# Kernel optimization log

Hardware: AMD Instinct MI355X
Metric: run time of the kernel (lower is better)

Reference implementation:

```python
import jax, jax.numpy as jnp
import numpy as np


def setup_inputs() -> dict:
    key = jax.random.key(0)
    k1, _ = jax.random.split(key)
    x = jax.random.normal(k1, (2, 16, 16, 16, 64), dtype=jnp.float32)
    gamma = jnp.ones((1,), dtype=jnp.float32)  # learned scalar (zeros at init; ones to make output nontrivial)
    return {"x": x, "gamma": gamma}


def reference(x, gamma):
    # x: (B, D, H, W, C); faithful to the Keras layer: flatten spatial dims,
    # energy = Q @ Q^T over the N=D*H*W axis, softmax(axis=-1), attn @ Q,
    # then gamma-scaled residual add.
    B, D, H, W, C = x.shape
    N = D * H * W
    q = x.reshape(B, N, C)                            # proj_query (B, N, C)
    energy = jnp.einsum('bnc,bmc->bnm', q, q)          # (B, N, N)
    attn = jax.nn.softmax(energy, axis=-1)
    out = jnp.einsum('bnm,bmc->bnc', attn, q)          # (B, N, C)
    out = out.reshape(B, D, H, W, C)
    return gamma * out + x
```

## Files before the change

### kernel.cpp

```cpp
#include <hip/hip_runtime.h>
#include <hip/hip_bf16.h>
#include <math.h>


#define NN 4096
#define CC 64
#define LOG2E 1.4426950408889634f

typedef __attribute__((ext_vector_type(4))) float f32x4;
typedef __attribute__((ext_vector_type(8))) short bf16x8;
typedef __attribute__((ext_vector_type(4))) short bf16x4;
typedef unsigned short u16;
typedef __attribute__((ext_vector_type(4))) u16 u16x4;
typedef __attribute__((ext_vector_type(2))) unsigned u32x2;

__device__ inline u16 f2bf(float f) {
  union { float f; unsigned u; } v; v.f = f;
  unsigned r = (v.u + 0x7fffu + ((v.u >> 16) & 1u)) >> 16;
  return (u16)r;
}
__device__ inline float bf2f(short h) {
  union { unsigned u; float f; } v;
  v.u = ((unsigned)(unsigned short)h) << 16;
  return v.f;
}
__device__ inline unsigned fbits(float f) {
  union { float f; unsigned u; } v; v.f = f;
  return v.u;
}
__device__ inline bf16x8 cvt8(f32x4 a, f32x4 b) {
  bf16x8 r;
  r[0] = (short)f2bf(a[0]); r[1] = (short)f2bf(a[1]);
  r[2] = (short)f2bf(a[2]); r[3] = (short)f2bf(a[3]);
  r[4] = (short)f2bf(b[0]); r[5] = (short)f2bf(b[1]);
  r[6] = (short)f2bf(b[2]); r[7] = (short)f2bf(b[3]);
  return r;
}

__global__ __launch_bounds__(256) void prep_kernel(const float* __restrict__ x,
                                                   u16* __restrict__ Qb,
                                                   u16* __restrict__ Vt) {
  __shared__ u16 t[64][68];
  const int id = blockIdx.x;
  const int s = id & 7;
  const int bk = id >> 3;
  const int b = bk >> 3;
  const int k = bk & 7;
  const int kb64 = s * 8 + k;
  const int n0 = kb64 * 64;
  const f32x4* x4 = (const f32x4*)(x + ((size_t)b * NN + n0) * CC);
  u16* qb = Qb + ((size_t)b * NN + n0) * CC;
#pragma unroll
  for (int it = 0; it < 4; ++it) {
    int idx4 = it * 256 + threadIdx.x;
    int i = idx4 >> 4, cg = idx4 & 15;
    f32x4 v = x4[idx4];
    u16x4 h;
    h[0] = f2bf(v[0]); h[1] = f2bf(v[1]); h[2] = f2bf(v[2]); h[3] = f2bf(v[3]);
    *(u16x4*)(qb + (size_t)idx4 * 4) = h;
    t[cg * 4 + 0][i] = h[0]; t[cg * 4 + 1][i] = h[1];
    t[cg * 4 + 2][i] = h[2]; t[cg * 4 + 3][i] = h[3];
  }
  __syncthreads();
  u16* vt = Vt + ((size_t)b * (NN / 64) + kb64) * (64 * 64);
#pragma unroll
  for (int it = 0; it < 4; ++it) {
    int idx4 = it * 256 + threadIdx.x;
    int c = idx4 >> 4, i4 = (idx4 & 15) * 4;
    u16x4 h = *(const u16x4*)(&t[c][i4]);
    *(u16x4*)(vt + c * 64 + i4) = h;
  }
}

template <int S>
__global__ __launch_bounds__(256, 4) void attn_split(
    const u16* __restrict__ Qb, const u16* __restrict__ Vt,
    u16* __restrict__ Opart, float* __restrict__ lpart) {
  constexpr int KPS = NN / S;
  constexpr int ITERS = KPS / 64;
  const int w = threadIdx.x >> 6;
  const int lane = threadIdx.x & 63;
  const int quad = lane >> 4, col = lane & 15;
  const int blk = blockIdx.x;
  const int b = blk / (64 * S);
  const int rg = (blk / S) & 63;
  const int s = blk % S;

  __shared__ u16 KT[2][64 * 64];
  __shared__ u16 VT[2][64 * 64];
  __shared__ u16 PB[4][16 * 64];

  const u16* Qbase = Qb + (size_t)b * NN * CC;
  const u16* Vbase = Vt + (size_t)b * NN * CC;
  const int row0 = rg * 64 + w * 16;

  bf16x8 qs0, qs1;
  float m_sc;
  {
    const u16* qp = Qbase + (size_t)(row0 + col) * CC + quad * 8;
    bf16x8 r0 = *(const bf16x8*)qp;
    bf16x8 r1 = *(const bf16x8*)(qp + 32);
    float msum = 0.f;
#pragma unroll
    for (int j = 0; j < 8; ++j) {
      float a0 = bf2f(r0[j]), a1 = bf2f(r1[j]);
      u16 h0 = f2bf(a0 * LOG2E), h1 = f2bf(a1 * LOG2E);
      qs0[j] = (short)h0; qs1[j] = (short)h1;
      msum += bf2f((short)h0) * a0 + bf2f((short)h1) * a1;
    }
    msum += __shfl_xor(msum, 16);
    msum += __shfl_xor(msum, 32);
    m_sc = msum;
  }

  f32x4 zero = {0.f, 0.f, 0.f, 0.f};
  f32x4 acc[4] = {zero, zero, zero, zero};
  float l_loc = 0.f;

  const int kk = lane >> 3;
  const int sw = (lane & 7) ^ kk;
  const u16* kptr = Qbase + (size_t)(s * KPS + w * 16 + kk) * CC + sw * 8;
  const u16* vptr = Vbase + ((size_t)(s * KPS >> 6) * 64 + (w * 16 + kk)) * 64 + sw * 8;

#define STAGE(p, kp, vp)                                                      \
  {                                                                           \
    _Pragma("unroll")                                                         \
    for (int g = 0; g < 2; ++g) {                                             \
      __builtin_amdgcn_global_load_lds(                                       \
          (const __attribute__((address_space(1))) unsigned*)((kp) + g * 512),\
          (__attribute__((address_space(3))) unsigned*)&KT[p][(w * 16 + g * 8) * 64], \
          16, 0, 0);                                                          \
      __builtin_amdgcn_global_load_lds(                                       \
          (const __attribute__((address_space(1))) unsigned*)((vp) + g * 512),\
          (__attribute__((address_space(3))) unsigned*)&VT[p][(w * 16 + g * 8) * 64], \
          16, 0, 0);                                                          \
    }                                                                         \
  }

  STAGE(0, kptr, vptr)
  const int cs = col & 7;
  u16* PBw = &PB[w][0];
#pragma unroll 2
  for (int i = 0; i < ITERS; ++i) {
    __syncthreads();
    const int p = i & 1;
    if (i + 1 < ITERS) STAGE(p ^ 1, kptr + 4096, vptr + 4096)
    kptr += 4096; vptr += 4096;

    f32x4 sx[4];
#pragma unroll
    for (int t = 0; t < 4; ++t) {
      bf16x8 ka = *(const bf16x8*)&KT[p][(t * 16 + col) * 64 + (quad ^ cs) * 8];
      bf16x8 kb = *(const bf16x8*)&KT[p][(t * 16 + col) * 64 + ((quad + 4) ^ cs) * 8];
      sx[t] = __builtin_amdgcn_mfma_f32_16x16x32_bf16(ka, qs0, zero, 0, 0, 0);
      sx[t] = __builtin_amdgcn_mfma_f32_16x16x32_bf16(kb, qs1, sx[t], 0, 0, 0);
    }
#pragma unroll
    for (int t = 0; t < 4; ++t) {
      f32x4 pv;
#pragma unroll
      for (int r = 0; r < 4; ++r) pv[r] = exp2f(sx[t][r] - m_sc);
      l_loc += pv[0] + pv[1] + pv[2] + pv[3];
      u32x2 d;
      d[0] = __builtin_amdgcn_perm(fbits(pv[1]), fbits(pv[0]), 0x07060302u);
      d[1] = __builtin_amdgcn_perm(fbits(pv[3]), fbits(pv[2]), 0x07060302u);
      *(u32x2*)&PBw[col * 64 + ((t * 2 + (quad >> 1)) ^ cs) * 8 + (quad & 1) * 4] = d;
    }
    bf16x8 pf0 = *(const bf16x8*)&PBw[col * 64 + (quad ^ cs) * 8];
    bf16x8 pf1 = *(const bf16x8*)&PBw[col * 64 + ((quad + 4) ^ cs) * 8];
#pragma unroll
    for (int cg = 0; cg < 4; ++cg) {
      bf16x8 va = *(const bf16x8*)&VT[p][(cg * 16 + col) * 64 + (quad ^ cs) * 8];
      bf16x8 vb = *(const bf16x8*)&VT[p][(cg * 16 + col) * 64 + ((quad + 4) ^ cs) * 8];
      acc[cg] = __builtin_amdgcn_mfma_f32_16x16x32_bf16(pf0, va, acc[cg], 0, 0, 0);
      acc[cg] = __builtin_amdgcn_mfma_f32_16x16x32_bf16(pf1, vb, acc[cg], 0, 0, 0);
    }
  }
#undef STAGE

  size_t pbase = (((size_t)(b * 64 + rg)) * S + s) * (64 * 64);
  size_t lbase = (((size_t)(b * 64 + rg)) * S + s) * 64;
  {
    float l = l_loc;
    l += __shfl_xor(l, 16);
    l += __shfl_xor(l, 32);
    if (quad == 0) lpart[lbase + w * 16 + col] = l;
  }
#pragma unroll
  for (int r = 0; r < 4; ++r) {
    int lr = w * 16 + quad * 4 + r;
    size_t o = pbase + (size_t)lr * 64;
    Opart[o + col]      = f2bf(acc[0][r]);
    Opart[o + col + 16] = f2bf(acc[1][r]);
    Opart[o + col + 32] = f2bf(acc[2][r]);
    Opart[o + col + 48] = f2bf(acc[3][r]);
  }
}

template <int S>
__global__ __launch_bounds__(256) void epi_kernel(
    const float* __restrict__ x, const float* __restrict__ gamma,
    const u16* __restrict__ Opart, const float* __restrict__ lpart,
    float* __restrict__ out) {
  int t = blockIdx.x * 256 + threadIdx.x;
  int cg = t & 15;
  int n = (t >> 4) & (NN - 1);
  int b = t >> 16;
  int rb = n >> 6, lr = n & 63;
  size_t obase = ((size_t)(b * 64 + rb) * S) * 4096 + (size_t)lr * 64 + cg * 4;
  size_t lbase = ((size_t)(b * 64 + rb) * S) * 64 + lr;
  f32x4 sO = {0.f, 0.f, 0.f, 0.f};
  float sL = 0.f;
#pragma unroll
  for (int s = 0; s < S; ++s) {
    u16x4 o4 = *(const u16x4*)(Opart + obase + (size_t)s * 4096);
    sL += lpart[lbase + s * 64];
    sO[0] += bf2f((short)o4[0]); sO[1] += bf2f((short)o4[1]);
    sO[2] += bf2f((short)o4[2]); sO[3] += bf2f((short)o4[3]);
  }
  size_t xi = (((size_t)b * NN + n) * CC + cg * 4);
  f32x4 xv = *(const f32x4*)(x + xi);
  float g = gamma[0], inv = 1.f / sL;
  f32x4 ov;
#pragma unroll
  for (int j = 0; j < 4; ++j) ov[j] = g * (sO[j] * inv) + xv[j];
  *(f32x4*)(((float*)out) + xi) = ov;
}

template <int WPB>
__global__ __launch_bounds__(WPB * 64, 4) void attn_fast(
    const float* __restrict__ x, const float* __restrict__ gamma,
    const u16* __restrict__ Qb, const u16* __restrict__ Vt,
    float* __restrict__ out) {
  const int w = threadIdx.x >> 6;
  const int lane = threadIdx.x & 63;
  const int quad = lane >> 4, col = lane & 15;
  const int b = blockIdx.x >> 8;
  const int tile = (blockIdx.x & 255) << 4;

  extern __shared__ char smem[];
  float* Osh = (float*)smem;
  float* lsh = Osh + WPB * 1024;
  u16* pl = (u16*)(lsh + WPB * 16) + w * 2176;

  const size_t xoff = (size_t)b * NN * CC;
  const u16* Qbase = Qb + xoff;
  const u16* Vbase = Vt + xoff;

  bf16x8 qf0 = *(const bf16x8*)(Qbase + (size_t)(tile + col) * CC + quad * 8);
  bf16x8 qf1 = *(const bf16x8*)(Qbase + (size_t)(tile + col) * CC + 32 + quad * 8);

  float msum = 0.f;
#pragma unroll
  for (int j = 0; j < 8; ++j) {
    float a = bf2f(qf0[j]), c = bf2f(qf1[j]);
    msum += a * a + c * c;
  }
  msum += __shfl_xor(msum, 16);
  msum += __shfl_xor(msum, 32);
  float m_i[4];
#pragma unroll
  for (int r = 0; r < 4; ++r) m_i[r] = __shfl(msum, quad * 4 + r);

  f32x4 zero = {0.f, 0.f, 0.f, 0.f};
  f32x4 acc[4] = {zero, zero, zero, zero};
  float l_i[4] = {0.f, 0.f, 0.f, 0.f};

  const int k0 = w * (NN / WPB);
#pragma unroll 2
  for (int kt = k0; kt < k0 + NN / WPB; kt += 64) {
    u16* plc = pl + ((kt >> 6) & 1) * 1088;
    f32x4 sx[4];
#pragma unroll
    for (int t = 0; t < 4; ++t) {
      const u16* kp = Qbase + (size_t)(kt + t * 16 + col) * CC + quad * 8;
      bf16x8 ka = *(const bf16x8*)kp;
      bf16x8 kb = *(const bf16x8*)(kp + 32);
      sx[t] = __builtin_amdgcn_mfma_f32_16x16x32_bf16(qf0, ka, zero, 0, 0, 0);
      sx[t] = __builtin_amdgcn_mfma_f32_16x16x32_bf16(qf1, kb, sx[t], 0, 0, 0);
    }
#pragma unroll
    for (int t = 0; t < 4; ++t) {
#pragma unroll
      for (int r = 0; r < 4; ++r) {
        float p = __expf(sx[t][r] - m_i[r]);
        l_i[r] += p;
        plc[(quad * 4 + r) * 68 + t * 16 + col] = f2bf(p);
      }
    }
    bf16x8 pf0 = *(const bf16x8*)(plc + col * 68 + quad * 8);
    bf16x8 pf1 = *(const bf16x8*)(plc + col * 68 + 32 + quad * 8);
#pragma unroll
    for (int cg = 0; cg < 4; ++cg) {
      const u16* vp = Vbase + (((size_t)(kt >> 6)) * 64 + cg * 16 + col) * 64 + quad * 8;
      bf16x8 v0 = *(const bf16x8*)vp;
      bf16x8 v1 = *(const bf16x8*)(vp + 32);
      acc[cg] = __builtin_amdgcn_mfma_f32_16x16x32_bf16(pf0, v0, acc[cg], 0, 0, 0);
      acc[cg] = __builtin_amdgcn_mfma_f32_16x16x32_bf16(pf1, v1, acc[cg], 0, 0, 0);
    }
  }

#pragma unroll
  for (int r = 0; r < 4; ++r)
#pragma unroll
    for (int off = 1; off < 16; off <<= 1) l_i[r] += __shfl_xor(l_i[r], off, 16);
#pragma unroll
  for (int r = 0; r < 4; ++r) {
    int row = quad * 4 + r;
    Osh[(w * 16 + row) * 64 + col]      = acc[0][r];
    Osh[(w * 16 + row) * 64 + col + 16] = acc[1][r];
    Osh[(w * 16 + row) * 64 + col + 32] = acc[2][r];
    Osh[(w * 16 + row) * 64 + col + 48] = acc[3][r];
    if (col == 0) lsh[w * 16 + row] = l_i[r];
  }
  __syncthreads();

  float g = gamma[0];
  for (int row = w; row < 16; row += WPB) {
    float L = 0.f, val = 0.f;
#pragma unroll
    for (int w2 = 0; w2 < WPB; ++w2) {
      L += lsh[w2 * 16 + row];
      val += Osh[(w2 * 16 + row) * 64 + lane];
    }
    size_t o = xoff + (size_t)(tile + row) * CC + lane;
    out[o] = g * (val / L) + x[o];
  }
}

template <int WPB>
__global__ __launch_bounds__(512) void attn_fb(const float* __restrict__ x,
                                               const float* __restrict__ gamma,
                                               float* __restrict__ out) {
  const int w = threadIdx.x >> 6;
  const int lane = threadIdx.x & 63;
  const int quad = lane >> 4, col = lane & 15;
  const int b = blockIdx.x >> 8;
  const int tile = (blockIdx.x & 255) << 4;

  extern __shared__ char smem[];
  float* Osh = (float*)smem;
  float* msh = Osh + WPB * 1024;
  float* lsh = msh + WPB * 16;
  u16* pl = (u16*)(lsh + WPB * 16) + w * 768;
  u16* vt = (u16*)(lsh + WPB * 16) + WPB * 768 + w * 2176;

  const size_t xoff = (size_t)b * NN * CC;
  const f32x4* x4 = (const f32x4*)(x + xoff);

  bf16x8 qf0, qf1;
  {
    int ri = (tile + col) * 16 + quad * 2;
    qf0 = cvt8(x4[ri], x4[ri + 1]);
    qf1 = cvt8(x4[ri + 8], x4[ri + 9]);
  }
  f32x4 zero = {0.f, 0.f, 0.f, 0.f};
  f32x4 acc0 = zero, acc1 = zero, acc2 = zero, acc3 = zero;
  float m_i[4], l_i[4];
#pragma unroll
  for (int r = 0; r < 4; ++r) { m_i[r] = -1e30f; l_i[r] = 0.f; }

  const int k0 = w * (NN / WPB);
  for (int kt = k0; kt < k0 + NN / WPB; kt += 32) {
    bf16x8 k00, k01, k10, k11;
    {
      int kb = (kt + col) * 16 + quad * 2;
      k00 = cvt8(x4[kb], x4[kb + 1]);
      k01 = cvt8(x4[kb + 8], x4[kb + 9]);
      k10 = cvt8(x4[kb + 256], x4[kb + 257]);
      k11 = cvt8(x4[kb + 264], x4[kb + 265]);
#pragma unroll
      for (int h = 0; h < 2; ++h) {
        bf16x8 va = h ? k10 : k00, vb = h ? k11 : k01;
        int base = (h * 16 + col) * 68 + quad * 8;
        *(bf16x4*)(vt + base) = __builtin_shufflevector(va, va, 0, 1, 2, 3);
        *(bf16x4*)(vt + base + 4) = __builtin_shufflevector(va, va, 4, 5, 6, 7);
        *(bf16x4*)(vt + base + 32) = __builtin_shufflevector(vb, vb, 0, 1, 2, 3);
        *(bf16x4*)(vt + base + 36) = __builtin_shufflevector(vb, vb, 4, 5, 6, 7);
      }
    }
    f32x4 s0 = zero, s1 = zero;
    s0 = __builtin_amdgcn_mfma_f32_16x16x32_bf16(qf0, k00, s0, 0, 0, 0);
    s0 = __builtin_amdgcn_mfma_f32_16x16x32_bf16(qf1, k01, s0, 0, 0, 0);
    s1 = __builtin_amdgcn_mfma_f32_16x16x32_bf16(qf0, k10, s1, 0, 0, 0);
    s1 = __builtin_amdgcn_mfma_f32_16x16x32_bf16(qf1, k11, s1, 0, 0, 0);

    float p0[4], p1[4], alpha[4];
#pragma unroll
    for (int r = 0; r < 4; ++r) {
      float mx = fmaxf(s0[r], s1[r]);
#pragma unroll
      for (int off = 1; off < 16; off <<= 1) mx = fmaxf(mx, __shfl_xor(mx, off, 16));
      float mn = fmaxf(m_i[r], mx);
      alpha[r] = __expf(m_i[r] - mn);
      p0[r] = __expf(s0[r] - mn);
      p1[r] = __expf(s1[r] - mn);
      float rs = p0[r] + p1[r];
#pragma unroll
      for (int off = 1; off < 16; off <<= 1) rs += __shfl_xor(rs, off, 16);
      l_i[r] = l_i[r] * alpha[r] + rs;
      m_i[r] = mn;
    }
#pragma unroll
    for (int r = 0; r < 4; ++r) {
      acc0[r] *= alpha[r]; acc1[r] *= alpha[r];
      acc2[r] *= alpha[r]; acc3[r] *= alpha[r];
    }
#pragma unroll
    for (int r = 0; r < 4; ++r) {
      pl[(quad * 4 + r) * 24 + col] = f2bf(p0[r]);
      pl[384 + (quad * 4 + r) * 24 + col] = f2bf(p1[r]);
    }
    bf16x8 pf = *(const bf16x8*)(pl + (quad >> 1) * 384 + col * 24 + (quad & 1) * 8);

    bf16x8 v0, v1, v2, v3;
#pragma unroll
    for (int j = 0; j < 8; ++j) {
      int rb = (quad * 8 + j) * 68 + col;
      v0[j] = (short)vt[rb];
      v1[j] = (short)vt[rb + 16];
      v2[j] = (short)vt[rb + 32];
      v3[j] = (short)vt[rb + 48];
    }
    acc0 = __builtin_amdgcn_mfma_f32_16x16x32_bf16(pf, v0, acc0, 0, 0, 0);
    acc1 = __builtin_amdgcn_mfma_f32_16x16x32_bf16(pf, v1, acc1, 0, 0, 0);
    acc2 = __builtin_amdgcn_mfma_f32_16x16x32_bf16(pf, v2, acc2, 0, 0, 0);
    acc3 = __builtin_amdgcn_mfma_f32_16x16x32_bf16(pf, v3, acc3, 0, 0, 0);
  }

#pragma unroll
  for (int r = 0; r < 4; ++r) {
    int row = quad * 4 + r;
    Osh[(w * 16 + row) * 64 + col] = acc0[r];
    Osh[(w * 16 + row) * 64 + col + 16] = acc1[r];
    Osh[(w * 16 + row) * 64 + col + 32] = acc2[r];
    Osh[(w * 16 + row) * 64 + col + 48] = acc3[r];
    if (col == 0) { msh[w * 16 + row] = m_i[r]; lsh[w * 16 + row] = l_i[r]; }
  }
  __syncthreads();

  float g = gamma[0];
  for (int row = w; row < 16; row += WPB) {
    float M = -1e30f;
#pragma unroll
    for (int w2 = 0; w2 < WPB; ++w2) M = fmaxf(M, msh[w2 * 16 + row]);
    float L = 0.f, val = 0.f;
#pragma unroll
    for (int w2 = 0; w2 < WPB; ++w2) {
      float e = __expf(msh[w2 * 16 + row] - M);
      L += lsh[w2 * 16 + row] * e;
      val += Osh[(w2 * 16 + row) * 64 + lane] * e;
    }
    size_t o = xoff + (size_t)(tile + row) * CC + lane;
    out[o] = g * (val / L) + x[o];
  }
}

extern "C" void kernel_launch(void* const* d_in, const int* in_sizes, int n_in,
                              void* d_out, int out_size, void* d_ws, size_t ws_size,
                              hipStream_t stream) {
  const float* x = (const float*)d_in[0];
  const float* gamma = (const float*)d_in[1];
  float* out = (float*)d_out;

  constexpr int S = 8;
  constexpr size_t kQV = (size_t)2 * 2 * NN * CC * sizeof(u16);
  constexpr size_t kOp = (size_t)2 * 64 * S * 64 * 64 * sizeof(u16);
  constexpr size_t kLp = (size_t)2 * 64 * S * 64 * sizeof(float);
  if (ws_size >= kQV + kOp + kLp) {
    u16* Qb = (u16*)d_ws;
    u16* Vt = Qb + (size_t)2 * NN * CC;
    u16* Opart = (u16*)((char*)d_ws + kQV);
    float* lpart = (float*)((char*)d_ws + kQV + kOp);
    prep_kernel<<<128, 256, 0, stream>>>(x, Qb, Vt);
    attn_split<S><<<2 * 64 * S, 256, 0, stream>>>(Qb, Vt, Opart, lpart);
    epi_kernel<S><<<(2 * NN * 16) / 256, 256, 0, stream>>>(x, gamma, Opart, lpart, out);
  } else if (ws_size >= kQV) {
    u16* Qb = (u16*)d_ws;
    u16* Vt = Qb + (size_t)2 * NN * CC;
    prep_kernel<<<128, 256, 0, stream>>>(x, Qb, Vt);
    constexpr int SM = 8 * 1024 * 4 + 8 * 16 * 4 + 8 * 2176 * 2;
    attn_fast<8><<<512, 512, SM, stream>>>(x, gamma, Qb, Vt, out);
  } else {
    constexpr int SM4 = 4 * (1024 + 32) * 4 + 4 * 768 * 2 + 4 * 2176 * 2;
    attn_fb<4><<<512, 256, SM4, stream>>>(x, gamma, out);
  }
}
```

Measured before the change: 82.16 us.

## Fuse prep, split attention and epilogue into one cooperative kernel with grid syncs

Replaces the three-kernel sequence (bf16 prep/transpose, split-K attention, reduction epilogue) with a single cooperative launch of 1024 blocks that runs the three phases separated by grid-wide barriers. The aim is to remove two kernel launch gaps and the tail/drain between dependent kernels. In exchange it adds two grid syncs, and the prep phase is spread thinly so that each block handles only 8 rows. If the cooperative launch fails, it falls back to the original three launches.

After: 283.4 us. 3.45x slower.

```diff
diff --git a/kernel.cpp b/kernel.cpp
--- a/kernel.cpp
+++ b/kernel.cpp
@@ -1,7 +1,10 @@
 #include <hip/hip_runtime.h>
 #include <hip/hip_bf16.h>
+#include <hip/hip_cooperative_groups.h>
 #include <math.h>
 
+
+namespace cg = cooperative_groups;
 
 #define NN 4096
 #define CC 64
@@ -35,6 +38,192 @@
   r[4] = (short)f2bf(b[0]); r[5] = (short)f2bf(b[1]);
   r[6] = (short)f2bf(b[2]); r[7] = (short)f2bf(b[3]);
   return r;
+}
+
+template <int S>
+__global__ __launch_bounds__(256, 4) void fused_kernel(
+    const float* __restrict__ x, const float* __restrict__ gamma,
+    u16* __restrict__ Qb, u16* __restrict__ Vt,
+    u16* __restrict__ Opart, float* __restrict__ lpart,
+    float* __restrict__ out) {
+  constexpr int KPS = NN / S;
+  constexpr int ITERS = KPS / 64;
+  __shared__ u16 KT[2][64 * 64];
+  __shared__ u16 VT[2][64 * 64];
+  __shared__ u16 PB[4][16 * 64];
+
+  {
+    u16(*t8)[8] = (u16(*)[8]) & KT[0][0];
+    const int g = blockIdx.x;
+    const int t = threadIdx.x;
+    const int n0 = g * 8;
+    const int b = n0 >> 12;
+    const int nb = n0 & (NN - 1);
+    if (t < 128) {
+      int i = t >> 4, cgi = t & 15;
+      f32x4 v = ((const f32x4*)x)[(size_t)g * 128 + t];
+      u16x4 h;
+      h[0] = f2bf(v[0]); h[1] = f2bf(v[1]); h[2] = f2bf(v[2]); h[3] = f2bf(v[3]);
+      *(u16x4*)(Qb + ((size_t)g * 128 + t) * 4) = h;
+      t8[cgi * 4 + 0][i] = h[0]; t8[cgi * 4 + 1][i] = h[1];
+      t8[cgi * 4 + 2][i] = h[2]; t8[cgi * 4 + 3][i] = h[3];
+    }
+    __syncthreads();
+    if (t < 64) {
+      int kb = nb >> 6, kw0 = nb & 63;
+      u16x4 a = *(const u16x4*)&t8[t][0];
+      u16x4 bq = *(const u16x4*)&t8[t][4];
+      u16* vt = Vt + ((size_t)b * (NN / 64) + kb) * 4096 + t * 64 + kw0;
+      *(u16x4*)vt = a;
+      *(u16x4*)(vt + 4) = bq;
+    }
+  }
+  cg::this_grid().sync();
+
+  {
+    const int w = threadIdx.x >> 6;
+    const int lane = threadIdx.x & 63;
+    const int quad = lane >> 4, col = lane & 15;
+    const int blk = blockIdx.x;
+    const int b = blk / (64 * S);
+    const int rg = (blk / S) & 63;
+    const int s = blk % S;
+
+    const u16* Qbase = Qb + (size_t)b * NN * CC;
+    const u16* Vbase = Vt + (size_t)b * NN * CC;
+    const int row0 = rg * 64 + w * 16;
+
+    bf16x8 qs0, qs1;
+    float m_sc;
+    {
+      const u16* qp = Qbase + (size_t)(row0 + col) * CC + quad * 8;
+      bf16x8 r0 = *(const bf16x8*)qp;
+      bf16x8 r1 = *(const bf16x8*)(qp + 32);
+      float msum = 0.f;
+#pragma unroll
+      for (int j = 0; j < 8; ++j) {
+        float a0 = bf2f(r0[j]), a1 = bf2f(r1[j]);
+        u16 h0 = f2bf(a0 * LOG2E), h1 = f2bf(a1 * LOG2E);
+        qs0[j] = (short)h0; qs1[j] = (short)h1;
+        msum += bf2f((short)h0) * a0 + bf2f((short)h1) * a1;
+      }
+      msum += __shfl_xor(msum, 16);
+      msum += __shfl_xor(msum, 32);
+      m_sc = msum;
+    }
+
+    f32x4 zero = {0.f, 0.f, 0.f, 0.f};
+    f32x4 acc[4] = {zero, zero, zero, zero};
+    float l_loc = 0.f;
+
+    const int kk = lane >> 3;
+    const int sw = (lane & 7) ^ kk;
+    const u16* kptr = Qbase + (size_t)(s * KPS + w * 16 + kk) * CC + sw * 8;
+    const u16* vptr = Vbase + ((size_t)(s * KPS >> 6) * 64 + (w * 16 + kk)) * 64 + sw * 8;
+
+#define STAGE(p, kp, vp)                                                      \
+  {                                                                           \
+    _Pragma("unroll")                                                         \
+    for (int g2 = 0; g2 < 2; ++g2) {                                          \
+      __builtin_amdgcn_global_load_lds(                                       \
+          (const __attribute__((address_space(1))) unsigned*)((kp) + g2 * 512),\
+          (__attribute__((address_space(3))) unsigned*)&KT[p][(w * 16 + g2 * 8) * 64], \
+          16, 0, 0);                                                          \
+      __builtin_amdgcn_global_load_lds(                                       \
+          (const __attribute__((address_space(1))) unsigned*)((vp) + g2 * 512),\
+          (__attribute__((address_space(3))) unsigned*)&VT[p][(w * 16 + g2 * 8) * 64], \
+          16, 0, 0);                                                          \
+    }                                                                         \
+  }
+
+    STAGE(0, kptr, vptr)
+    const int cs = col & 7;
+    u16* PBw = &PB[w][0];
+#pragma unroll 2
+    for (int i = 0; i < ITERS; ++i) {
+      __syncthreads();
+      const int p = i & 1;
+      if (i + 1 < ITERS) STAGE(p ^ 1, kptr + 4096, vptr + 4096)
+      kptr += 4096; vptr += 4096;
+
+      f32x4 sx[4];
+#pragma unroll
+      for (int t = 0; t < 4; ++t) {
+        bf16x8 ka = *(const bf16x8*)&KT[p][(t * 16 + col) * 64 + (quad ^ cs) * 8];
+        bf16x8 kb = *(const bf16x8*)&KT[p][(t * 16 + col) * 64 + ((quad + 4) ^ cs) * 8];
+        sx[t] = __builtin_amdgcn_mfma_f32_16x16x32_bf16(ka, qs0, zero, 0, 0, 0);
+        sx[t] = __builtin_amdgcn_mfma_f32_16x16x32_bf16(kb, qs1, sx[t], 0, 0, 0);
+      }
+#pragma unroll
+      for (int t = 0; t < 4; ++t) {
+        f32x4 pv;
+#pragma unroll
+        for (int r = 0; r < 4; ++r) pv[r] = exp2f(sx[t][r] - m_sc);
+        l_loc += pv[0] + pv[1] + pv[2] + pv[3];
+        u32x2 d;
+        d[0] = __builtin_amdgcn_perm(fbits(pv[1]), fbits(pv[0]), 0x07060302u);
+        d[1] = __builtin_amdgcn_perm(fbits(pv[3]), fbits(pv[2]), 0x07060302u);
+        *(u32x2*)&PBw[col * 64 + ((t * 2 + (quad >> 1)) ^ cs) * 8 + (quad & 1) * 4] = d;
+      }
+      bf16x8 pf0 = *(const bf16x8*)&PBw[col * 64 + (quad ^ cs) * 8];
+      bf16x8 pf1 = *(const bf16x8*)&PBw[col * 64 + ((quad + 4) ^ cs) * 8];
+#pragma unroll
+      for (int cgi = 0; cgi < 4; ++cgi) {
+        bf16x8 va = *(const bf16x8*)&VT[p][(cgi * 16 + col) * 64 + (quad ^ cs) * 8];
+        bf16x8 vb = *(const bf16x8*)&VT[p][(cgi * 16 + col) * 64 + ((quad + 4) ^ cs) * 8];
+        acc[cgi] = __builtin_amdgcn_mfma_f32_16x16x32_bf16(pf0, va, acc[cgi], 0, 0, 0);
+        acc[cgi] = __builtin_amdgcn_mfma_f32_16x16x32_bf16(pf1, vb, acc[cgi], 0, 0, 0);
+      }
+    }
+#undef STAGE
+
+    size_t pbase = (((size_t)(b * 64 + rg)) * S + s) * (64 * 64);
+    size_t lbase = (((size_t)(b * 64 + rg)) * S + s) * 64;
+    {
+      float l = l_loc;
+      l += __shfl_xor(l, 16);
+      l += __shfl_xor(l, 32);
+      if (quad == 0) lpart[lbase + w * 16 + col] = l;
+    }
+#pragma unroll
+    for (int r = 0; r < 4; ++r) {
+      int lr = w * 16 + quad * 4 + r;
+      size_t o = pbase + (size_t)lr * 64;
+      Opart[o + col]      = f2bf(acc[0][r]);
+      Opart[o + col + 16] = f2bf(acc[1][r]);
+      Opart[o + col + 32] = f2bf(acc[2][r]);
+      Opart[o + col + 48] = f2bf(acc[3][r]);
+    }
+  }
+  cg::this_grid().sync();
+
+  {
+    int tid = blockIdx.x * 256 + threadIdx.x;
+    if (tid < 2 * NN * 16) {
+      int cgi = tid & 15;
+      int n = (tid >> 4) & (NN - 1);
+      int b = tid >> 16;
+      int rb = n >> 6, lr = n & 63;
+      size_t obase = ((size_t)(b * 64 + rb) * S) * 4096 + (size_t)lr * 64 + cgi * 4;
+      size_t lbase = ((size_t)(b * 64 + rb) * S) * 64 + lr;
+      f32x4 sO = {0.f, 0.f, 0.f, 0.f};
+      float sL = 0.f;
+#pragma unroll
+      for (int s = 0; s < S; ++s) {
+        u16x4 o4 = *(const u16x4*)(Opart + obase + (size_t)s * 4096);
+        sL += lpart[lbase + s * 64];
+        sO[0] += bf2f((short)o4[0]); sO[1] += bf2f((short)o4[1]);
+        sO[2] += bf2f((short)o4[2]); sO[3] += bf2f((short)o4[3]);
+      }
+      size_t xi = (((size_t)b * NN + n) * CC + cgi * 4);
+      f32x4 xv = *(const f32x4*)(x + xi);
+      float g = gamma[0], inv = 1.f / sL;
+      f32x4 ov;
+#pragma unroll
+      for (int j = 0; j < 4; ++j) ov[j] = g * (sO[j] * inv) + xv[j];
+      *(f32x4*)(out + xi) = ov;
+    }
+  }
 }
 
 __global__ __launch_bounds__(256) void prep_kernel(const float* __restrict__ x,
@@ -53,13 +242,13 @@
 #pragma unroll
   for (int it = 0; it < 4; ++it) {
     int idx4 = it * 256 + threadIdx.x;
-    int i = idx4 >> 4, cg = idx4 & 15;
+    int i = idx4 >> 4, cgi = idx4 & 15;
     f32x4 v = x4[idx4];
     u16x4 h;
     h[0] = f2bf(v[0]); h[1] = f2bf(v[1]); h[2] = f2bf(v[2]); h[3] = f2bf(v[3]);
     *(u16x4*)(qb + (size_t)idx4 * 4) = h;
-    t[cg * 4 + 0][i] = h[0]; t[cg * 4 + 1][i] = h[1];
-    t[cg * 4 + 2][i] = h[2]; t[cg * 4 + 3][i] = h[3];
+    t[cgi * 4 + 0][i] = h[0]; t[cgi * 4 + 1][i] = h[1];
+    t[cgi * 4 + 2][i] = h[2]; t[cgi * 4 + 3][i] = h[3];
   }
   __syncthreads();
   u16* vt = Vt + ((size_t)b * (NN / 64) + kb64) * (64 * 64);
@@ -169,11 +358,11 @@
     bf16x8 pf0 = *(const bf16x8*)&PBw[col * 64 + (quad ^ cs) * 8];
     bf16x8 pf1 = *(const bf16x8*)&PBw[col * 64 + ((quad + 4) ^ cs) * 8];
 #pragma unroll
-    for (int cg = 0; cg < 4; ++cg) {
-      bf16x8 va = *(const bf16x8*)&VT[p][(cg * 16 + col) * 64 + (quad ^ cs) * 8];
-      bf16x8 vb = *(const bf16x8*)&VT[p][(cg * 16 + col) * 64 + ((quad + 4) ^ cs) * 8];
-      acc[cg] = __builtin_amdgcn_mfma_f32_16x16x32_bf16(pf0, va, acc[cg], 0, 0, 0);
-      acc[cg] = __builtin_amdgcn_mfma_f32_16x16x32_bf16(pf1, vb, acc[cg], 0, 0, 0);
+    for (int cgi = 0; cgi < 4; ++cgi) {
+      bf16x8 va = *(const bf16x8*)&VT[p][(cgi * 16 + col) * 64 + (quad ^ cs) * 8];
+      bf16x8 vb = *(const bf16x8*)&VT[p][(cgi * 16 + col) * 64 + ((quad + 4) ^ cs) * 8];
+      acc[cgi] = __builtin_amdgcn_mfma_f32_16x16x32_bf16(pf0, va, acc[cgi], 0, 0, 0);
+      acc[cgi] = __builtin_amdgcn_mfma_f32_16x16x32_bf16(pf1, vb, acc[cgi], 0, 0, 0);
     }
   }
 #undef STAGE
@@ -203,11 +392,11 @@
     const u16* __restrict__ Opart, const float* __restrict__ lpart,
     float* __restrict__ out) {
   int t = blockIdx.x * 256 + threadIdx.x;
-  int cg = t & 15;
+  int cgi = t & 15;
   int n = (t >> 4) & (NN - 1);
   int b = t >> 16;
   int rb = n >> 6, lr = n & 63;
-  size_t obase = ((size_t)(b * 64 + rb) * S) * 4096 + (size_t)lr * 64 + cg * 4;
+  size_t obase = ((size_t)(b * 64 + rb) * S) * 4096 + (size_t)lr * 64 + cgi * 4;
   size_t lbase = ((size_t)(b * 64 + rb) * S) * 64 + lr;
   f32x4 sO = {0.f, 0.f, 0.f, 0.f};
   float sL = 0.f;
@@ -218,13 +407,13 @@
     sO[0] += bf2f((short)o4[0]); sO[1] += bf2f((short)o4[1]);
     sO[2] += bf2f((short)o4[2]); sO[3] += bf2f((short)o4[3]);
   }
-  size_t xi = (((size_t)b * NN + n) * CC + cg * 4);
+  size_t xi = (((size_t)b * NN + n) * CC + cgi * 4);
   f32x4 xv = *(const f32x4*)(x + xi);
   float g = gamma[0], inv = 1.f / sL;
   f32x4 ov;
 #pragma unroll
   for (int j = 0; j < 4; ++j) ov[j] = g * (sO[j] * inv) + xv[j];
-  *(f32x4*)(((float*)out) + xi) = ov;
+  *(f32x4*)(out + xi) = ov;
 }
 
 template <int WPB>
@@ -291,12 +480,12 @@
     bf16x8 pf0 = *(const bf16x8*)(plc + col * 68 + quad * 8);
     bf16x8 pf1 = *(const bf16x8*)(plc + col * 68 + 32 + quad * 8);
 #pragma unroll
-    for (int cg = 0; cg < 4; ++cg) {
-      const u16* vp = Vbase + (((size_t)(kt >> 6)) * 64 + cg * 16 + col) * 64 + quad * 8;
+    for (int cgi = 0; cgi < 4; ++cgi) {
+      const u16* vp = Vbase + (((size_t)(kt >> 6)) * 64 + cgi * 16 + col) * 64 + quad * 8;
       bf16x8 v0 = *(const bf16x8*)vp;
       bf16x8 v1 = *(const bf16x8*)(vp + 32);
-      acc[cg] = __builtin_amdgcn_mfma_f32_16x16x32_bf16(pf0, v0, acc[cg], 0, 0, 0);
-      acc[cg] = __builtin_amdgcn_mfma_f32_16x16x32_bf16(pf1, v1, acc[cg], 0, 0, 0);
+      acc[cgi] = __builtin_amdgcn_mfma_f32_16x16x32_bf16(pf0, v0, acc[cgi], 0, 0, 0);
+      acc[cgi] = __builtin_amdgcn_mfma_f32_16x16x32_bf16(pf1, v1, acc[cgi], 0, 0, 0);
     }
   }
 
@@ -472,9 +661,21 @@
     u16* Vt = Qb + (size_t)2 * NN * CC;
     u16* Opart = (u16*)((char*)d_ws + kQV);
     float* lpart = (float*)((char*)d_ws + kQV + kOp);
-    prep_kernel<<<128, 256, 0, stream>>>(x, Qb, Vt);
-    attn_split<S><<<2 * 64 * S, 256, 0, stream>>>(Qb, Vt, Opart, lpart);
-    epi_kernel<S><<<(2 * NN * 16) / 256, 256, 0, stream>>>(x, gamma, Opart, lpart, out);
+    const float* xa = x; const float* ga = gamma;
+    u16* qa = Qb; u16* va = Vt; u16* oa = Opart; float* la = lpart;
+    float* outa = out;
+    void* args[] = {(void*)&xa, (void*)&ga, (void*)&qa, (void*)&va,
+                    (void*)&oa, (void*)&la, (void*)&outa};
+    hipError_t err = hipLaunchCooperativeKernel(
+        reinterpret_cast<void*>(fused_kernel<S>), dim3(2 * 64 * S), dim3(256),
+        args, 0, stream);
+    if (err != hipSuccess) {
+      (void)hipGetLastError();
+      prep_kernel<<<128, 256, 0, stream>>>(x, Qb, Vt);
+      attn_split<S><<<2 * 64 * S, 256, 0, stream>>>(Qb, Vt, Opart, lpart);
+      epi_kernel<S><<<(2 * NN * 16) / 256, 256, 0, stream>>>(x, gamma, Opart,
+                                                             lpart, out);
+    }
   } else if (ws_size >= kQV) {
     u16* Qb = (u16*)d_ws;
     u16* Vt = Qb + (size_t)2 * NN * CC;
```

## Switch split attention to 32x32x16 MFMA with 128-row tiles and register P exchange

Applied to the files above, without the earlier changes.

The split-K attention kernel now uses 32x32x16 bf16 MFMA instead of 16x16x32. Each wave owns 32 query rows, so a block covers 128 rows. The probability tile is repacked in registers with a cross-half shuffle, removing the LDS round trip through the PB buffer. The split count rises from 8 to 16 to keep the grid size the same, the loop is fully unrolled, and the epilogue indexing is updated to match. The aim is higher MFMA efficiency and fewer LDS writes and reads per K/V tile, at the cost of more registers and more partial outputs to reduce.

Measured after the change: 88.77 us. 1.08x slower.

```diff
diff --git a/kernel.cpp b/kernel.cpp
--- a/kernel.cpp
+++ b/kernel.cpp
@@ -8,11 +8,12 @@
 #define LOG2E 1.4426950408889634f
 
 typedef __attribute__((ext_vector_type(4))) float f32x4;
+typedef __attribute__((ext_vector_type(16))) float f32x16;
 typedef __attribute__((ext_vector_type(8))) short bf16x8;
 typedef __attribute__((ext_vector_type(4))) short bf16x4;
 typedef unsigned short u16;
 typedef __attribute__((ext_vector_type(4))) u16 u16x4;
-typedef __attribute__((ext_vector_type(2))) unsigned u32x2;
+typedef unsigned long long ull;
 
 __device__ inline u16 f2bf(float f) {
   union { float f; unsigned u; } v; v.f = f;
@@ -42,24 +43,21 @@
                                                    u16* __restrict__ Vt) {
   __shared__ u16 t[64][68];
   const int id = blockIdx.x;
-  const int s = id & 7;
-  const int bk = id >> 3;
-  const int b = bk >> 3;
-  const int k = bk & 7;
-  const int kb64 = s * 8 + k;
+  const int b = id >> 6;
+  const int kb64 = id & 63;
   const int n0 = kb64 * 64;
   const f32x4* x4 = (const f32x4*)(x + ((size_t)b * NN + n0) * CC);
   u16* qb = Qb + ((size_t)b * NN + n0) * CC;
 #pragma unroll
   for (int it = 0; it < 4; ++it) {
     int idx4 = it * 256 + threadIdx.x;
-    int i = idx4 >> 4, cg = idx4 & 15;
+    int i = idx4 >> 4, cgi = idx4 & 15;
     f32x4 v = x4[idx4];
     u16x4 h;
     h[0] = f2bf(v[0]); h[1] = f2bf(v[1]); h[2] = f2bf(v[2]); h[3] = f2bf(v[3]);
     *(u16x4*)(qb + (size_t)idx4 * 4) = h;
-    t[cg * 4 + 0][i] = h[0]; t[cg * 4 + 1][i] = h[1];
-    t[cg * 4 + 2][i] = h[2]; t[cg * 4 + 3][i] = h[3];
+    t[cgi * 4 + 0][i] = h[0]; t[cgi * 4 + 1][i] = h[1];
+    t[cgi * 4 + 2][i] = h[2]; t[cgi * 4 + 3][i] = h[3];
   }
   __syncthreads();
   u16* vt = Vt + ((size_t)b * (NN / 64) + kb64) * (64 * 64);
@@ -73,48 +71,50 @@
 }
 
 template <int S>
-__global__ __launch_bounds__(256, 4) void attn_split(
+__global__ __launch_bounds__(256, 4) void attn32(
     const u16* __restrict__ Qb, const u16* __restrict__ Vt,
     u16* __restrict__ Opart, float* __restrict__ lpart) {
   constexpr int KPS = NN / S;
   constexpr int ITERS = KPS / 64;
   const int w = threadIdx.x >> 6;
   const int lane = threadIdx.x & 63;
-  const int quad = lane >> 4, col = lane & 15;
+  const int qr = lane & 31;
+  const int hl = lane >> 5;
   const int blk = blockIdx.x;
-  const int b = blk / (64 * S);
-  const int rg = (blk / S) & 63;
+  const int b = blk / (32 * S);
+  const int rg = (blk / S) & 31;
   const int s = blk % S;
 
   __shared__ u16 KT[2][64 * 64];
   __shared__ u16 VT[2][64 * 64];
-  __shared__ u16 PB[4][16 * 64];
 
   const u16* Qbase = Qb + (size_t)b * NN * CC;
   const u16* Vbase = Vt + (size_t)b * NN * CC;
-  const int row0 = rg * 64 + w * 16;
-
-  bf16x8 qs0, qs1;
+  const int row0 = rg * 128 + w * 32;
+
+  bf16x8 qf[4];
   float m_sc;
   {
-    const u16* qp = Qbase + (size_t)(row0 + col) * CC + quad * 8;
-    bf16x8 r0 = *(const bf16x8*)qp;
-    bf16x8 r1 = *(const bf16x8*)(qp + 32);
+    const u16* qp = Qbase + (size_t)(row0 + qr) * CC + hl * 8;
     float msum = 0.f;
 #pragma unroll
-    for (int j = 0; j < 8; ++j) {
-      float a0 = bf2f(r0[j]), a1 = bf2f(r1[j]);
-      u16 h0 = f2bf(a0 * LOG2E), h1 = f2bf(a1 * LOG2E);
-      qs0[j] = (short)h0; qs1[j] = (short)h1;
-      msum += bf2f((short)h0) * a0 + bf2f((short)h1) * a1;
-    }
-    msum += __shfl_xor(msum, 16);
+    for (int ks = 0; ks < 4; ++ks) {
+      bf16x8 r = *(const bf16x8*)(qp + 16 * ks);
+#pragma unroll
+      for (int j = 0; j < 8; ++j) {
+        float a = bf2f(r[j]);
+        u16 h = f2bf(a * LOG2E);
+        qf[ks][j] = (short)h;
+        msum += bf2f((short)h) * a;
+      }
+    }
     msum += __shfl_xor(msum, 32);
     m_sc = msum;
   }
 
-  f32x4 zero = {0.f, 0.f, 0.f, 0.f};
-  f32x4 acc[4] = {zero, zero, zero, zero};
+  f32x16 acc0, acc1;
+#pragma unroll
+  for (int r = 0; r < 16; ++r) { acc0[r] = 0.f; acc1[r] = 0.f; }
   float l_loc = 0.f;
 
   const int kk = lane >> 3;
@@ -122,78 +122,90 @@
   const u16* kptr = Qbase + (size_t)(s * KPS + w * 16 + kk) * CC + sw * 8;
   const u16* vptr = Vbase + ((size_t)(s * KPS >> 6) * 64 + (w * 16 + kk)) * 64 + sw * 8;
 
-#define STAGE(p, kp, vp)                                                      \
+#define STAGE(p, kp_, vp_)                                                    \
   {                                                                           \
     _Pragma("unroll")                                                         \
     for (int g = 0; g < 2; ++g) {                                             \
       __builtin_amdgcn_global_load_lds(                                       \
-          (const __attribute__((address_space(1))) unsigned*)((kp) + g * 512),\
+          (const __attribute__((address_space(1))) unsigned*)((kp_) + g * 512),\
           (__attribute__((address_space(3))) unsigned*)&KT[p][(w * 16 + g * 8) * 64], \
           16, 0, 0);                                                          \
       __builtin_amdgcn_global_load_lds(                                       \
-          (const __attribute__((address_space(1))) unsigned*)((vp) + g * 512),\
+          (const __attribute__((address_space(1))) unsigned*)((vp_) + g * 512),\
           (__attribute__((address_space(3))) unsigned*)&VT[p][(w * 16 + g * 8) * 64], \
           16, 0, 0);                                                          \
     }                                                                         \
   }
 
   STAGE(0, kptr, vptr)
-  const int cs = col & 7;
-  u16* PBw = &PB[w][0];
-#pragma unroll 2
+  const int q7 = qr & 7;
+#pragma unroll
   for (int i = 0; i < ITERS; ++i) {
     __syncthreads();
     const int p = i & 1;
     if (i + 1 < ITERS) STAGE(p ^ 1, kptr + 4096, vptr + 4096)
     kptr += 4096; vptr += 4096;
 
-    f32x4 sx[4];
-#pragma unroll
-    for (int t = 0; t < 4; ++t) {
-      bf16x8 ka = *(const bf16x8*)&KT[p][(t * 16 + col) * 64 + (quad ^ cs) * 8];
-      bf16x8 kb = *(const bf16x8*)&KT[p][(t * 16 + col) * 64 + ((quad + 4) ^ cs) * 8];
-      sx[t] = __builtin_amdgcn_mfma_f32_16x16x32_bf16(ka, qs0, zero, 0, 0, 0);
-      sx[t] = __builtin_amdgcn_mfma_f32_16x16x32_bf16(kb, qs1, sx[t], 0, 0, 0);
-    }
-#pragma unroll
-    for (int t = 0; t < 4; ++t) {
-      f32x4 pv;
-#pragma unroll
-      for (int r = 0; r < 4; ++r) pv[r] = exp2f(sx[t][r] - m_sc);
-      l_loc += pv[0] + pv[1] + pv[2] + pv[3];
-      u32x2 d;
-      d[0] = __builtin_amdgcn_perm(fbits(pv[1]), fbits(pv[0]), 0x07060302u);
-      d[1] = __builtin_amdgcn_perm(fbits(pv[3]), fbits(pv[2]), 0x07060302u);
-      *(u32x2*)&PBw[col * 64 + ((t * 2 + (quad >> 1)) ^ cs) * 8 + (quad & 1) * 4] = d;
-    }
-    bf16x8 pf0 = *(const bf16x8*)&PBw[col * 64 + (quad ^ cs) * 8];
-    bf16x8 pf1 = *(const bf16x8*)&PBw[col * 64 + ((quad + 4) ^ cs) * 8];
-#pragma unroll
-    for (int cg = 0; cg < 4; ++cg) {
-      bf16x8 va = *(const bf16x8*)&VT[p][(cg * 16 + col) * 64 + (quad ^ cs) * 8];
-      bf16x8 vb = *(const bf16x8*)&VT[p][(cg * 16 + col) * 64 + ((quad + 4) ^ cs) * 8];
-      acc[cg] = __builtin_amdgcn_mfma_f32_16x16x32_bf16(pf0, va, acc[cg], 0, 0, 0);
-      acc[cg] = __builtin_amdgcn_mfma_f32_16x16x32_bf16(pf1, vb, acc[cg], 0, 0, 0);
+    ull packs[2][4];
+#pragma unroll
+    for (int kt2 = 0; kt2 < 2; ++kt2) {
+      f32x16 sx;
+#pragma unroll
+      for (int r = 0; r < 16; ++r) sx[r] = 0.f;
+      const int krow = kt2 * 32 + qr;
+#pragma unroll
+      for (int ks = 0; ks < 4; ++ks) {
+        int pos = (2 * ks + hl) ^ (krow & 7);
+        bf16x8 ka = *(const bf16x8*)&KT[p][krow * 64 + pos * 8];
+        sx = __builtin_amdgcn_mfma_f32_32x32x16_bf16(ka, qf[ks], sx, 0, 0, 0);
+      }
+#pragma unroll
+      for (int rr = 0; rr < 4; ++rr) {
+        float p0 = exp2f(sx[4 * rr + 0] - m_sc);
+        float p1 = exp2f(sx[4 * rr + 1] - m_sc);
+        float p2 = exp2f(sx[4 * rr + 2] - m_sc);
+        float p3 = exp2f(sx[4 * rr + 3] - m_sc);
+        l_loc += (p0 + p1) + (p2 + p3);
+        unsigned d0 = __builtin_amdgcn_perm(fbits(p1), fbits(p0), 0x07060302u);
+        unsigned d1 = __builtin_amdgcn_perm(fbits(p3), fbits(p2), 0x07060302u);
+        packs[kt2][rr] = (ull)d0 | ((ull)d1 << 32);
+      }
+    }
+
+#pragma unroll
+    for (int kp = 0; kp < 4; ++kp) {
+      const int kt2 = kp >> 1;
+      ull own = packs[kt2][2 * (kp & 1) + hl];
+      ull oth = __shfl_xor(packs[kt2][2 * (kp & 1) + 1 - hl], 32);
+      ull lo = hl ? oth : own;
+      ull hi = hl ? own : oth;
+      bf16x8 pf;
+      ((ull*)&pf)[0] = lo;
+      ((ull*)&pf)[1] = hi;
+#pragma unroll
+      for (int ct = 0; ct < 2; ++ct) {
+        int vrow = ct * 32 + qr;
+        int pos = (2 * kp + hl) ^ (vrow & 7);
+        bf16x8 vb = *(const bf16x8*)&VT[p][vrow * 64 + pos * 8];
+        if (ct == 0)
+          acc0 = __builtin_amdgcn_mfma_f32_32x32x16_bf16(pf, vb, acc0, 0, 0, 0);
+        else
+          acc1 = __builtin_amdgcn_mfma_f32_32x32x16_bf16(pf, vb, acc1, 0, 0, 0);
+      }
     }
   }
 #undef STAGE
-
-  size_t pbase = (((size_t)(b * 64 + rg)) * S + s) * (64 * 64);
-  size_t lbase = (((size_t)(b * 64 + rg)) * S + s) * 64;
-  {
-    float l = l_loc;
-    l += __shfl_xor(l, 16);
-    l += __shfl_xor(l, 32);
-    if (quad == 0) lpart[lbase + w * 16 + col] = l;
-  }
-#pragma unroll
-  for (int r = 0; r < 4; ++r) {
-    int lr = w * 16 + quad * 4 + r;
-    size_t o = pbase + (size_t)lr * 64;
-    Opart[o + col]      = f2bf(acc[0][r]);
-    Opart[o + col + 16] = f2bf(acc[1][r]);
-    Opart[o + col + 32] = f2bf(acc[2][r]);
-    Opart[o + col + 48] = f2bf(acc[3][r]);
+  (void)q7;
+
+  l_loc += __shfl_xor(l_loc, 32);
+  size_t pbase = ((size_t)((b * 32 + rg) * S + s)) * (128 * 64);
+  size_t lbase = ((size_t)((b * 32 + rg) * S + s)) * 128;
+  if (hl == 0) lpart[lbase + w * 32 + qr] = l_loc;
+#pragma unroll
+  for (int reg = 0; reg < 16; ++reg) {
+    int lr = w * 32 + (reg & 3) + 8 * (reg >> 2) + 4 * hl;
+    Opart[pbase + (size_t)lr * 64 + qr]      = f2bf(acc0[reg]);
+    Opart[pbase + (size_t)lr * 64 + 32 + qr] = f2bf(acc1[reg]);
   }
 }
 
@@ -203,28 +215,28 @@
     const u16* __restrict__ Opart, const float* __restrict__ lpart,
     float* __restrict__ out) {
   int t = blockIdx.x * 256 + threadIdx.x;
-  int cg = t & 15;
+  int cgi = t & 15;
   int n = (t >> 4) & (NN - 1);
   int b = t >> 16;
-  int rb = n >> 6, lr = n & 63;
-  size_t obase = ((size_t)(b * 64 + rb) * S) * 4096 + (size_t)lr * 64 + cg * 4;
-  size_t lbase = ((size_t)(b * 64 + rb) * S) * 64 + lr;
+  int rg = n >> 7, lr = n & 127;
+  size_t obase = ((size_t)(b * 32 + rg) * S) * (128 * 64) + (size_t)lr * 64 + cgi * 4;
+  size_t lbase = ((size_t)(b * 32 + rg) * S) * 128 + lr;
   f32x4 sO = {0.f, 0.f, 0.f, 0.f};
   float sL = 0.f;
 #pragma unroll
   for (int s = 0; s < S; ++s) {
-    u16x4 o4 = *(const u16x4*)(Opart + obase + (size_t)s * 4096);
-    sL += lpart[lbase + s * 64];
+    u16x4 o4 = *(const u16x4*)(Opart + obase + (size_t)s * (128 * 64));
+    sL += lpart[lbase + s * 128];
     sO[0] += bf2f((short)o4[0]); sO[1] += bf2f((short)o4[1]);
     sO[2] += bf2f((short)o4[2]); sO[3] += bf2f((short)o4[3]);
   }
-  size_t xi = (((size_t)b * NN + n) * CC + cg * 4);
+  size_t xi = (((size_t)b * NN + n) * CC + cgi * 4);
   f32x4 xv = *(const f32x4*)(x + xi);
   float g = gamma[0], inv = 1.f / sL;
   f32x4 ov;
 #pragma unroll
   for (int j = 0; j < 4; ++j) ov[j] = g * (sO[j] * inv) + xv[j];
-  *(f32x4*)(((float*)out) + xi) = ov;
+  *(f32x4*)(out + xi) = ov;
 }
 
 template <int WPB>
@@ -291,12 +303,12 @@
     bf16x8 pf0 = *(const bf16x8*)(plc + col * 68 + quad * 8);
     bf16x8 pf1 = *(const bf16x8*)(plc + col * 68 + 32 + quad * 8);
 #pragma unroll
-    for (int cg = 0; cg < 4; ++cg) {
-      const u16* vp = Vbase + (((size_t)(kt >> 6)) * 64 + cg * 16 + col) * 64 + quad * 8;
+    for (int cgi = 0; cgi < 4; ++cgi) {
+      const u16* vp = Vbase + (((size_t)(kt >> 6)) * 64 + cgi * 16 + col) * 64 + quad * 8;
       bf16x8 v0 = *(const bf16x8*)vp;
       bf16x8 v1 = *(const bf16x8*)(vp + 32);
-      acc[cg] = __builtin_amdgcn_mfma_f32_16x16x32_bf16(pf0, v0, acc[cg], 0, 0, 0);
-      acc[cg] = __builtin_amdgcn_mfma_f32_16x16x32_bf16(pf1, v1, acc[cg], 0, 0, 0);
+      acc[cgi] = __builtin_amdgcn_mfma_f32_16x16x32_bf16(pf0, v0, acc[cgi], 0, 0, 0);
+      acc[cgi] = __builtin_amdgcn_mfma_f32_16x16x32_bf16(pf1, v1, acc[cgi], 0, 0, 0);
     }
   }
 
@@ -463,17 +475,17 @@
   const float* gamma = (const float*)d_in[1];
   float* out = (float*)d_out;
 
-  constexpr int S = 8;
+  constexpr int S = 16;
   constexpr size_t kQV = (size_t)2 * 2 * NN * CC * sizeof(u16);
-  constexpr size_t kOp = (size_t)2 * 64 * S * 64 * 64 * sizeof(u16);
-  constexpr size_t kLp = (size_t)2 * 64 * S * 64 * sizeof(float);
+  constexpr size_t kOp = (size_t)2 * 32 * S * 128 * 64 * sizeof(u16);
+  constexpr size_t kLp = (size_t)2 * 32 * S * 128 * sizeof(float);
   if (ws_size >= kQV + kOp + kLp) {
     u16* Qb = (u16*)d_ws;
     u16* Vt = Qb + (size_t)2 * NN * CC;
     u16* Opart = (u16*)((char*)d_ws + kQV);
     float* lpart = (float*)((char*)d_ws + kQV + kOp);
     prep_kernel<<<128, 256, 0, stream>>>(x, Qb, Vt);
-    attn_split<S><<<2 * 64 * S, 256, 0, stream>>>(Qb, Vt, Opart, lpart);
+    attn32<S><<<2 * 32 * S, 256, 0, stream>>>(Qb, Vt, Opart, lpart);
     epi_kernel<S><<<(2 * NN * 16) / 256, 256, 0, stream>>>(x, gamma, Opart, lpart, out);
   } else if (ws_size >= kQV) {
     u16* Qb = (u16*)d_ws;
```

## Fuse split-K epilogue into attention kernel via last-block atomic counter

Applied to the files above, without the earlier changes.

Removes the separate epilogue kernel. Each split block now fences and atomically increments a per-row-group counter, and the last block to finish reduces the partial O and l buffers and writes the gamma-scaled residual output. The counters are zeroed inside the prep kernel, which also switches to a simpler block-to-tile mapping. This saves a kernel launch and its inter-kernel gap, at the cost of threadfences, atomics and a serialized reduction tail in the last-arriving blocks.

Result: slower. 266.3 us (+224.1%).

```diff
diff --git a/kernel.cpp b/kernel.cpp
--- a/kernel.cpp
+++ b/kernel.cpp
@@ -39,27 +39,26 @@
 
 __global__ __launch_bounds__(256) void prep_kernel(const float* __restrict__ x,
                                                    u16* __restrict__ Qb,
-                                                   u16* __restrict__ Vt) {
+                                                   u16* __restrict__ Vt,
+                                                   int* __restrict__ cnt) {
   __shared__ u16 t[64][68];
   const int id = blockIdx.x;
-  const int s = id & 7;
-  const int bk = id >> 3;
-  const int b = bk >> 3;
-  const int k = bk & 7;
-  const int kb64 = s * 8 + k;
+  if (id == 0 && threadIdx.x < 128) cnt[threadIdx.x] = 0;
+  const int b = id >> 6;
+  const int kb64 = id & 63;
   const int n0 = kb64 * 64;
   const f32x4* x4 = (const f32x4*)(x + ((size_t)b * NN + n0) * CC);
   u16* qb = Qb + ((size_t)b * NN + n0) * CC;
 #pragma unroll
   for (int it = 0; it < 4; ++it) {
     int idx4 = it * 256 + threadIdx.x;
-    int i = idx4 >> 4, cg = idx4 & 15;
+    int i = idx4 >> 4, cgi = idx4 & 15;
     f32x4 v = x4[idx4];
     u16x4 h;
     h[0] = f2bf(v[0]); h[1] = f2bf(v[1]); h[2] = f2bf(v[2]); h[3] = f2bf(v[3]);
     *(u16x4*)(qb + (size_t)idx4 * 4) = h;
-    t[cg * 4 + 0][i] = h[0]; t[cg * 4 + 1][i] = h[1];
-    t[cg * 4 + 2][i] = h[2]; t[cg * 4 + 3][i] = h[3];
+    t[cgi * 4 + 0][i] = h[0]; t[cgi * 4 + 1][i] = h[1];
+    t[cgi * 4 + 2][i] = h[2]; t[cgi * 4 + 3][i] = h[3];
   }
   __syncthreads();
   u16* vt = Vt + ((size_t)b * (NN / 64) + kb64) * (64 * 64);
@@ -74,8 +73,10 @@
 
 template <int S>
 __global__ __launch_bounds__(256, 4) void attn_split(
+    const float* __restrict__ x, const float* __restrict__ gamma,
     const u16* __restrict__ Qb, const u16* __restrict__ Vt,
-    u16* __restrict__ Opart, float* __restrict__ lpart) {
+    u16* __restrict__ Opart, float* __restrict__ lpart,
+    int* __restrict__ cnt, float* __restrict__ out) {
   constexpr int KPS = NN / S;
   constexpr int ITERS = KPS / 64;
   const int w = threadIdx.x >> 6;
@@ -169,11 +170,11 @@
     bf16x8 pf0 = *(const bf16x8*)&PBw[col * 64 + (quad ^ cs) * 8];
     bf16x8 pf1 = *(const bf16x8*)&PBw[col * 64 + ((quad + 4) ^ cs) * 8];
 #pragma unroll
-    for (int cg = 0; cg < 4; ++cg) {
-      bf16x8 va = *(const bf16x8*)&VT[p][(cg * 16 + col) * 64 + (quad ^ cs) * 8];
-      bf16x8 vb = *(const bf16x8*)&VT[p][(cg * 16 + col) * 64 + ((quad + 4) ^ cs) * 8];
-      acc[cg] = __builtin_amdgcn_mfma_f32_16x16x32_bf16(pf0, va, acc[cg], 0, 0, 0);
-      acc[cg] = __builtin_amdgcn_mfma_f32_16x16x32_bf16(pf1, vb, acc[cg], 0, 0, 0);
+    for (int cgi = 0; cgi < 4; ++cgi) {
+      bf16x8 va = *(const bf16x8*)&VT[p][(cgi * 16 + col) * 64 + (quad ^ cs) * 8];
+      bf16x8 vb = *(const bf16x8*)&VT[p][(cgi * 16 + col) * 64 + ((quad + 4) ^ cs) * 8];
+      acc[cgi] = __builtin_amdgcn_mfma_f32_16x16x32_bf16(pf0, va, acc[cgi], 0, 0, 0);
+      acc[cgi] = __builtin_amdgcn_mfma_f32_16x16x32_bf16(pf1, vb, acc[cgi], 0, 0, 0);
     }
   }
 #undef STAGE
@@ -195,36 +196,43 @@
     Opart[o + col + 32] = f2bf(acc[2][r]);
     Opart[o + col + 48] = f2bf(acc[3][r]);
   }
-}
-
-template <int S>
-__global__ __launch_bounds__(256) void epi_kernel(
-    const float* __restrict__ x, const float* __restrict__ gamma,
-    const u16* __restrict__ Opart, const float* __restrict__ lpart,
-    float* __restrict__ out) {
-  int t = blockIdx.x * 256 + threadIdx.x;
-  int cg = t & 15;
-  int n = (t >> 4) & (NN - 1);
-  int b = t >> 16;
-  int rb = n >> 6, lr = n & 63;
-  size_t obase = ((size_t)(b * 64 + rb) * S) * 4096 + (size_t)lr * 64 + cg * 4;
-  size_t lbase = ((size_t)(b * 64 + rb) * S) * 64 + lr;
-  f32x4 sO = {0.f, 0.f, 0.f, 0.f};
-  float sL = 0.f;
-#pragma unroll
-  for (int s = 0; s < S; ++s) {
-    u16x4 o4 = *(const u16x4*)(Opart + obase + (size_t)s * 4096);
-    sL += lpart[lbase + s * 64];
-    sO[0] += bf2f((short)o4[0]); sO[1] += bf2f((short)o4[1]);
-    sO[2] += bf2f((short)o4[2]); sO[3] += bf2f((short)o4[3]);
-  }
-  size_t xi = (((size_t)b * NN + n) * CC + cg * 4);
-  f32x4 xv = *(const f32x4*)(x + xi);
-  float g = gamma[0], inv = 1.f / sL;
-  f32x4 ov;
-#pragma unroll
-  for (int j = 0; j < 4; ++j) ov[j] = g * (sO[j] * inv) + xv[j];
-  *(f32x4*)(((float*)out) + xi) = ov;
+
+  __threadfence();
+  volatile int* flag = (volatile int*)&PB[0][0];
+  if (threadIdx.x == 0) {
+    int old = atomicAdd(&cnt[b * 64 + rg], 1);
+    *flag = (old == S - 1);
+  }
+  __syncthreads();
+  if (*flag) {
+    __threadfence();
+    float g = gamma[0];
+    size_t gb = ((size_t)(b * 64 + rg)) * S;
+#pragma unroll
+    for (int c = 0; c < 4; ++c) {
+      int chunk = c * 256 + threadIdx.x;
+      int lr = chunk >> 4, cgi = chunk & 15;
+      size_t obase = gb * 4096 + (size_t)lr * 64 + cgi * 4;
+      size_t lb2 = gb * 64 + lr;
+      f32x4 sO = {0.f, 0.f, 0.f, 0.f};
+      float sL = 0.f;
+#pragma unroll
+      for (int s2 = 0; s2 < S; ++s2) {
+        u16x4 o4 = *(const u16x4*)(Opart + obase + (size_t)s2 * 4096);
+        sL += lpart[lb2 + s2 * 64];
+        sO[0] += bf2f((short)o4[0]); sO[1] += bf2f((short)o4[1]);
+        sO[2] += bf2f((short)o4[2]); sO[3] += bf2f((short)o4[3]);
+      }
+      int n = rg * 64 + lr;
+      size_t xi = (((size_t)b * NN + n) * CC + cgi * 4);
+      f32x4 xv = *(const f32x4*)(x + xi);
+      float inv = 1.f / sL;
+      f32x4 ov;
+#pragma unroll
+      for (int j = 0; j < 4; ++j) ov[j] = g * (sO[j] * inv) + xv[j];
+      *(f32x4*)(out + xi) = ov;
+    }
+  }
 }
 
 template <int WPB>
@@ -291,12 +299,12 @@
     bf16x8 pf0 = *(const bf16x8*)(plc + col * 68 + quad * 8);
     bf16x8 pf1 = *(const bf16x8*)(plc + col * 68 + 32 + quad * 8);
 #pragma unroll
-    for (int cg = 0; cg < 4; ++cg) {
-      const u16* vp = Vbase + (((size_t)(kt >> 6)) * 64 + cg * 16 + col) * 64 + quad * 8;
+    for (int cgi = 0; cgi < 4; ++cgi) {
+      const u16* vp = Vbase + (((size_t)(kt >> 6)) * 64 + cgi * 16 + col) * 64 + quad * 8;
       bf16x8 v0 = *(const bf16x8*)vp;
       bf16x8 v1 = *(const bf16x8*)(vp + 32);
-      acc[cg] = __builtin_amdgcn_mfma_f32_16x16x32_bf16(pf0, v0, acc[cg], 0, 0, 0);
-      acc[cg] = __builtin_amdgcn_mfma_f32_16x16x32_bf16(pf1, v1, acc[cg], 0, 0, 0);
+      acc[cgi] = __builtin_amdgcn_mfma_f32_16x16x32_bf16(pf0, v0, acc[cgi], 0, 0, 0);
+      acc[cgi] = __builtin_amdgcn_mfma_f32_16x16x32_bf16(pf1, v1, acc[cgi], 0, 0, 0);
     }
   }
 
@@ -467,18 +475,22 @@
   constexpr size_t kQV = (size_t)2 * 2 * NN * CC * sizeof(u16);
   constexpr size_t kOp = (size_t)2 * 64 * S * 64 * 64 * sizeof(u16);
   constexpr size_t kLp = (size_t)2 * 64 * S * 64 * sizeof(float);
-  if (ws_size >= kQV + kOp + kLp) {
+  constexpr size_t kCnt = 128 * sizeof(int);
+  if (ws_size >= kQV + kOp + kLp + kCnt) {
     u16* Qb = (u16*)d_ws;
     u16* Vt = Qb + (size_t)2 * NN * CC;
     u16* Opart = (u16*)((char*)d_ws + kQV);
     float* lpart = (float*)((char*)d_ws + kQV + kOp);
-    prep_kernel<<<128, 256, 0, stream>>>(x, Qb, Vt);
-    attn_split<S><<<2 * 64 * S, 256, 0, stream>>>(Qb, Vt, Opart, lpart);
-    epi_kernel<S><<<(2 * NN * 16) / 256, 256, 0, stream>>>(x, gamma, Opart, lpart, out);
+    int* cnt = (int*)((char*)d_ws + kQV + kOp + kLp);
+    prep_kernel<<<128, 256, 0, stream>>>(x, Qb, Vt, cnt);
+    attn_split<S><<<2 * 64 * S, 256, 0, stream>>>(x, gamma, Qb, Vt, Opart,
+                                                  lpart, cnt, out);
   } else if (ws_size >= kQV) {
     u16* Qb = (u16*)d_ws;
     u16* Vt = Qb + (size_t)2 * NN * CC;
-    prep_kernel<<<128, 256, 0, stream>>>(x, Qb, Vt);
+    int* cnt = nullptr;
+    (void)cnt;
+    prep_kernel<<<128, 256, 0, stream>>>(x, Qb, Vt, (int*)(Qb));
     constexpr int SM = 8 * 1024 * 4 + 8 * 16 * 4 + 8 * 2176 * 2;
     attn_fast<8><<<512, 512, SM, stream>>>(x, gamma, Qb, Vt, out);
   } else {
```
